# Optimization experiments

Measured on AMD Instinct MI355X. Metric: run time of the kernel, lower is better.

The kernel has to match this reference:

```python
import jax, jax.numpy as jnp
import numpy as np

N_SRC, N_TGT, K = 16384, 65536, 8      # coarse nodes, fine nodes, IDW neighbours per target
C, C_SKIP, S, HID = 16, 2, 32, 64      # mv channels (d_model), skip mv channels, scalars, MLP hidden
MV = 16                                # PGA multivector blade dimension


def setup_inputs() -> dict:
    key = jax.random.key(0)
    ks = jax.random.split(key, 11)
    E = N_TGT * K
    return {
        'mv_src': jax.random.normal(ks[0], (N_SRC, C, MV), jnp.float32),
        'mv_skip': jax.random.normal(ks[1], (N_TGT, C_SKIP, MV), jnp.float32),
        'sc_src': jax.random.normal(ks[2], (N_SRC, S), jnp.float32),
        'sc_skip': jax.random.normal(ks[3], (N_TGT, S), jnp.float32),
        'pos_src': jax.random.uniform(ks[4], (N_SRC, 3), jnp.float32),
        'pos_tgt': jax.random.uniform(ks[5], (N_TGT, 3), jnp.float32),
        'interp_source': jax.random.randint(ks[6], (E,), 0, N_SRC, dtype=jnp.int32),
        # every target receives exactly K source contributions (sorted, like torch_geometric knn edges)
        'interp_target': jnp.repeat(jnp.arange(N_TGT, dtype=jnp.int32), K),
        'W1_mv': jax.random.normal(ks[7], (C + C_SKIP, HID), jnp.float32) / np.float32(np.sqrt(C + C_SKIP)),
        'W2_mv': jax.random.normal(ks[8], (HID, C), jnp.float32) / np.float32(np.sqrt(HID)),
        'W1_s': jax.random.normal(ks[9], (2 * S, HID), jnp.float32) / np.float32(np.sqrt(2 * S)),
        'b1_s': jnp.zeros((HID,), jnp.float32),
        'W2_s': jax.random.normal(ks[10], (HID, S), jnp.float32) / np.float32(np.sqrt(HID)),
        'b2_s': jnp.zeros((S,), jnp.float32),
    }


def _interp(mv_src, mv_skip, sc_src, sc_skip, pos_src, pos_tgt,
            interp_source, interp_target, W1_mv, W2_mv, W1_s, b1_s, W2_s, b2_s):
    # --- inverse-distance-weighted interpolation (gather -> weight -> scatter-sum) ---
    pos_diff = pos_src[interp_source] - pos_tgt[interp_target]            # [E,3]
    d2 = jnp.clip(jnp.sum(pos_diff * pos_diff, axis=-1), 1e-16)           # [E]
    w = 1.0 / d2                                                          # IDW weight
    denom = jax.ops.segment_sum(w, interp_target, num_segments=N_TGT)     # [N_tgt]
    mv = jax.ops.segment_sum(mv_src[interp_source] * w[:, None, None],
                             interp_target, num_segments=N_TGT) / denom[:, None, None]
    sc = jax.ops.segment_sum(sc_src[interp_source] * w[:, None],
                             interp_target, num_segments=N_TGT) / denom[:, None]
    # --- skip concat (torch.cat dim=-2 for multivectors, dim=-1 for scalars) ---
    mv = jnp.concatenate((mv, mv_skip), axis=-2)                          # [N_tgt, C+C_SKIP, 16]
    sc = jnp.concatenate((sc, sc_skip), axis=-1)                          # [N_tgt, 2S]
    # --- equivariant MLP: channel-mixing linear on multivectors (blade-wise), gated scalar path ---
    mv_h = jnp.einsum('nci,ch->nhi', mv, W1_mv)                           # [N_tgt, HID, 16]
    sc_h = jax.nn.gelu(sc @ W1_s + b1_s)                                  # [N_tgt, HID]
    mv_o = jnp.einsum('nhi,hc->nci', mv_h, W2_mv)                         # [N_tgt, C, 16]
    sc_o = sc_h @ W2_s + b2_s                                             # [N_tgt, S]
    return mv_o, sc_o


def reference(mv_src, mv_skip, sc_src, sc_skip, pos_src, pos_tgt,
              interp_source, interp_target, W1_mv, W2_mv, W1_s, b1_s, W2_s, b2_s):
    return _interp(mv_src, mv_skip, sc_src, sc_skip, pos_src, pos_tgt,
                   interp_source, interp_target, W1_mv, W2_mv, W1_s, b1_s, W2_s, b2_s)
```

## Files before the change

### kernel.cpp

```cpp
#include <hip/hip_runtime.h>
#include <hip/hip_fp16.h>

#define N_SRC 16384
#define N_TGT 65536
#define KNN 8
#define CMV 16
#define CSKIP 2
#define SSC 32
#define HID 64
#define MVD 16

#define OUT_MV_ELEMS (N_TGT * CMV * MVD)
#define PROJ_OFFSET 512

__device__ __forceinline__ float gelu_tanh(float x) {
    const float k0 = 0.7978845608028654f;
    const float k1 = 0.044715f;
    float yy = k0 * (x + k1 * x * x * x);
    return 0.5f * x * (1.0f + tanhf(yy));
}

__global__ __launch_bounds__(256) void kA_preproject(
        const float* __restrict__ mv_src,
        const float* __restrict__ W1_mv,
        const float* __restrict__ W2_mv,
        float* __restrict__ ws) {
    __shared__ float sWeff[CMV][MVD];
    int tid = threadIdx.x;
    {
        int c = tid >> 4, d = tid & 15;
        float a = 0.f;
        #pragma unroll 8
        for (int h = 0; h < HID; ++h)
            a = fmaf(W1_mv[c * HID + h], W2_mv[h * MVD + d], a);
        sWeff[c][d] = a;
    }
    if (blockIdx.x == 0 && tid < 32) {
        int j = tid >> 4, d = tid & 15;
        float a = 0.f;
        #pragma unroll 8
        for (int h = 0; h < HID; ++h)
            a = fmaf(W1_mv[(CMV + j) * HID + h], W2_mv[h * MVD + d], a);
        ws[j * MVD + d] = a;
    }
    __syncthreads();

    int lane = tid & 63;
    int d = lane >> 2, q = lane & 3;
    float wcol[CMV];
    #pragma unroll
    for (int c = 0; c < CMV; ++c) wcol[c] = sWeff[c][d];

    __half* proj = (__half*)(ws + PROJ_OFFSET);
    int wid = (int)((blockIdx.x * blockDim.x + tid) >> 6);
    int nw  = (int)((gridDim.x * blockDim.x) >> 6);
    for (int s = wid; s < N_SRC; s += nw) {
        const float* row = mv_src + (size_t)s * 256;
        float4 o = make_float4(0.f, 0.f, 0.f, 0.f);
        #pragma unroll
        for (int c = 0; c < CMV; ++c) {
            float4 v = *(const float4*)(row + c * 16 + q * 4);
            o.x = fmaf(v.x, wcol[c], o.x);
            o.y = fmaf(v.y, wcol[c], o.y);
            o.z = fmaf(v.z, wcol[c], o.z);
            o.w = fmaf(v.w, wcol[c], o.w);
        }
        union { __half2 h[2]; uint2 u; } P;
        P.h[0] = __floats2half2_rn(o.x, o.y);
        P.h[1] = __floats2half2_rn(o.z, o.w);
        *(uint2*)(proj + (size_t)s * 256 + lane * 4) = P.u;
    }
}

__global__ __launch_bounds__(256, 6) void kB_mv(
        const float* __restrict__ ws,
        const float* __restrict__ mv_skip,
        const float* __restrict__ pos_src,
        const float* __restrict__ pos_tgt,
        const int*   __restrict__ isrc,
        float* __restrict__ out) {
    int tid = threadIdx.x;
    int lane = tid & 63;
    int d = lane >> 2, q = lane & 3;
    float wsk0 = ws[d];
    float wsk1 = ws[MVD + d];
    const __half* proj = (const __half*)(ws + PROJ_OFFSET);

    int wid = (int)((blockIdx.x * blockDim.x + tid) >> 6);
    int t0 = wid * 8;

    #pragma unroll
    for (int pp = 0; pp < 4; ++pp) {
        int tA = t0 + pp * 2, tB = tA + 1;
        float wA = 0.f, wB = 0.f; int sA = 0, sB = 0;
        if (lane < KNN) {
            sA = isrc[tA * KNN + lane];
            sB = isrc[tB * KNN + lane];
            float ax = pos_src[sA * 3 + 0] - pos_tgt[tA * 3 + 0];
            float ay = pos_src[sA * 3 + 1] - pos_tgt[tA * 3 + 1];
            float az = pos_src[sA * 3 + 2] - pos_tgt[tA * 3 + 2];
            float bx = pos_src[sB * 3 + 0] - pos_tgt[tB * 3 + 0];
            float by = pos_src[sB * 3 + 1] - pos_tgt[tB * 3 + 1];
            float bz = pos_src[sB * 3 + 2] - pos_tgt[tB * 3 + 2];
            float dA = fmaxf(ax * ax + ay * ay + az * az, 1e-16f);
            float dB = fmaxf(bx * bx + by * by + bz * bz, 1e-16f);
            wA = 1.0f / dA;
            wB = 1.0f / dB;
        }
        float denA = wA, denB = wB;
        denA += __shfl_xor(denA, 1); denB += __shfl_xor(denB, 1);
        denA += __shfl_xor(denA, 2); denB += __shfl_xor(denB, 2);
        denA += __shfl_xor(denA, 4); denB += __shfl_xor(denB, 4);
        float wnA = wA / denA, wnB = wB / denB;

        uint2 g[16];
        #pragma unroll
        for (int k = 0; k < KNN; ++k) {
            int sk = __builtin_amdgcn_readlane(sA, k);
            g[k] = *(const uint2*)(proj + (size_t)sk * 256 + lane * 4);
        }
        #pragma unroll
        for (int k = 0; k < KNN; ++k) {
            int sk = __builtin_amdgcn_readlane(sB, k);
            g[8 + k] = *(const uint2*)(proj + (size_t)sk * 256 + lane * 4);
        }

        float4 accA = make_float4(0.f, 0.f, 0.f, 0.f);
        float4 accB = make_float4(0.f, 0.f, 0.f, 0.f);
        #pragma unroll
        for (int k = 0; k < KNN; ++k) {
            float wk = __uint_as_float(
                __builtin_amdgcn_readlane(__float_as_uint(wnA), k));
            union { uint2 u; __half2 h[2]; } P; P.u = g[k];
            float2 lo = __half22float2(P.h[0]);
            float2 hi = __half22float2(P.h[1]);
            accA.x = fmaf(wk, lo.x, accA.x);
            accA.y = fmaf(wk, lo.y, accA.y);
            accA.z = fmaf(wk, hi.x, accA.z);
            accA.w = fmaf(wk, hi.y, accA.w);
        }
        #pragma unroll
        for (int k = 0; k < KNN; ++k) {
            float wk = __uint_as_float(
                __builtin_amdgcn_readlane(__float_as_uint(wnB), k));
            union { uint2 u; __half2 h[2]; } P; P.u = g[8 + k];
            float2 lo = __half22float2(P.h[0]);
            float2 hi = __half22float2(P.h[1]);
            accB.x = fmaf(wk, lo.x, accB.x);
            accB.y = fmaf(wk, lo.y, accB.y);
            accB.z = fmaf(wk, hi.x, accB.z);
            accB.w = fmaf(wk, hi.y, accB.w);
        }

        {
            const float4 u0 = *(const float4*)(mv_skip + (size_t)tA * 32 + q * 4);
            const float4 u1 = *(const float4*)(mv_skip + (size_t)tA * 32 + 16 + q * 4);
            float4 o;
            o.x = accA.x + fmaf(wsk0, u0.x, wsk1 * u1.x);
            o.y = accA.y + fmaf(wsk0, u0.y, wsk1 * u1.y);
            o.z = accA.z + fmaf(wsk0, u0.z, wsk1 * u1.z);
            o.w = accA.w + fmaf(wsk0, u0.w, wsk1 * u1.w);
            *(float4*)(out + (size_t)tA * 256 + lane * 4) = o;
        }
        {
            const float4 u0 = *(const float4*)(mv_skip + (size_t)tB * 32 + q * 4);
            const float4 u1 = *(const float4*)(mv_skip + (size_t)tB * 32 + 16 + q * 4);
            float4 o;
            o.x = accB.x + fmaf(wsk0, u0.x, wsk1 * u1.x);
            o.y = accB.y + fmaf(wsk0, u0.y, wsk1 * u1.y);
            o.z = accB.z + fmaf(wsk0, u0.z, wsk1 * u1.z);
            o.w = accB.w + fmaf(wsk0, u0.w, wsk1 * u1.w);
            *(float4*)(out + (size_t)tB * 256 + lane * 4) = o;
        }
    }
}

__global__ __launch_bounds__(256) void kBf_mv(
        const float* __restrict__ mv_src,
        const float* __restrict__ mv_skip,
        const float* __restrict__ pos_src,
        const float* __restrict__ pos_tgt,
        const int*   __restrict__ isrc,
        const float* __restrict__ W1_mv,
        const float* __restrict__ W2_mv,
        float* __restrict__ out) {
    __shared__ float sWeff[CMV + CSKIP][MVD];
    __shared__ float stage[4][256];
    int tid = threadIdx.x;
    for (int e = tid; e < (CMV + CSKIP) * MVD; e += 256) {
        int c = e >> 4, d = e & 15;
        float a = 0.f;
        #pragma unroll 8
        for (int h = 0; h < HID; ++h)
            a = fmaf(W1_mv[c * HID + h], W2_mv[h * MVD + d], a);
        sWeff[c][d] = a;
    }
    __syncthreads();

    int lane = tid & 63, wv = tid >> 6;
    int d = lane >> 2, q = lane & 3;
    float wcol[CMV + CSKIP];
    #pragma unroll
    for (int c = 0; c < CMV + CSKIP; ++c) wcol[c] = sWeff[c][d];

    int wid = (int)((blockIdx.x * blockDim.x + tid) >> 6);
    int nw  = (int)((gridDim.x * blockDim.x) >> 6);
    for (int t = wid; t < N_TGT; t += nw) {
        float w = 0.f; int src = 0;
        if (lane < KNN) {
            src = isrc[t * KNN + lane];
            float dx = pos_src[src * 3 + 0] - pos_tgt[t * 3 + 0];
            float dy = pos_src[src * 3 + 1] - pos_tgt[t * 3 + 1];
            float dz = pos_src[src * 3 + 2] - pos_tgt[t * 3 + 2];
            float d2 = fmaxf(dx * dx + dy * dy + dz * dz, 1e-16f);
            w = 1.0f / d2;
        }
        float denom = w;
        denom += __shfl_xor(denom, 1);
        denom += __shfl_xor(denom, 2);
        denom += __shfl_xor(denom, 4);
        denom = __shfl(denom, 0);
        float invd = 1.0f / denom;

        float4 acc = make_float4(0.f, 0.f, 0.f, 0.f);
        #pragma unroll
        for (int k = 0; k < KNN; ++k) {
            int   sk = __builtin_amdgcn_readlane(src, k);
            float wk = __uint_as_float(__builtin_amdgcn_readlane(__float_as_uint(w), k));
            float4 v = *(const float4*)(mv_src + (size_t)sk * 256 + lane * 4);
            acc.x = fmaf(wk, v.x, acc.x);
            acc.y = fmaf(wk, v.y, acc.y);
            acc.z = fmaf(wk, v.z, acc.z);
            acc.w = fmaf(wk, v.w, acc.w);
        }
        asm volatile("" ::: "memory");
        *(float4*)&stage[wv][lane * 4] = acc;
        asm volatile("s_waitcnt lgkmcnt(0)" ::: "memory");
        __builtin_amdgcn_sched_barrier(0);

        float4 o = make_float4(0.f, 0.f, 0.f, 0.f);
        #pragma unroll
        for (int c = 0; c < CMV; ++c) {
            float4 v = *(const float4*)&stage[wv][c * 16 + q * 4];
            o.x = fmaf(v.x, wcol[c], o.x);
            o.y = fmaf(v.y, wcol[c], o.y);
            o.z = fmaf(v.z, wcol[c], o.z);
            o.w = fmaf(v.w, wcol[c], o.w);
        }
        const float4 u0 = *(const float4*)(mv_skip + (size_t)t * 32 + q * 4);
        const float4 u1 = *(const float4*)(mv_skip + (size_t)t * 32 + 16 + q * 4);
        float4 r;
        r.x = fmaf(o.x, invd, fmaf(wcol[16], u0.x, wcol[17] * u1.x));
        r.y = fmaf(o.y, invd, fmaf(wcol[16], u0.y, wcol[17] * u1.y));
        r.z = fmaf(o.z, invd, fmaf(wcol[16], u0.z, wcol[17] * u1.z));
        r.w = fmaf(o.w, invd, fmaf(wcol[16], u0.w, wcol[17] * u1.w));
        *(float4*)(out + (size_t)t * 256 + lane * 4) = r;
    }
}

__global__ __launch_bounds__(256) void kC_scalar(
        const float* __restrict__ sc_src,
        const float* __restrict__ sc_skip,
        const float* __restrict__ pos_src,
        const float* __restrict__ pos_tgt,
        const int*   __restrict__ isrc,
        const float* __restrict__ W1_s,
        const float* __restrict__ b1_s,
        const float* __restrict__ W2_s,
        const float* __restrict__ b2_s,
        float* __restrict__ out) {
    __shared__ float sW1[HID * HID];
    __shared__ float sW2T[SSC][68];
    __shared__ float sXT[HID][68];
    __shared__ float sH[64][68];
    __shared__ float swgt[64][9];
    __shared__ int   ssrcl[64][9];
    __shared__ float sb1[HID], sb2[SSC];

    int tid = threadIdx.x;
    #pragma unroll
    for (int r = 0; r < 4; ++r) {
        float4 v = *(const float4*)(W1_s + (r * 256 + tid) * 4);
        *(float4*)&sW1[(r * 256 + tid) * 4] = v;
    }
    for (int e = tid; e < HID * SSC; e += 256) {
        int h = e >> 5, s = e & 31;
        sW2T[s][h] = W2_s[e];
    }
    if (tid < HID) sb1[tid] = b1_s[tid];
    else if (tid < HID + SSC) sb2[tid - HID] = b2_s[tid - HID];

    int t0 = blockIdx.x * 64;
    if (tid < 64) {
        int t = t0 + tid;
        float ptx = pos_tgt[t * 3 + 0], pty = pos_tgt[t * 3 + 1], ptz = pos_tgt[t * 3 + 2];
        int4 e0 = *(const int4*)(isrc + t * KNN);
        int4 e1 = *(const int4*)(isrc + t * KNN + 4);
        int sk[KNN] = {e0.x, e0.y, e0.z, e0.w, e1.x, e1.y, e1.z, e1.w};
        float wk[KNN];
        float denom = 0.f;
        #pragma unroll
        for (int k = 0; k < KNN; ++k) {
            int s = sk[k];
            float dx = pos_src[s * 3 + 0] - ptx;
            float dy = pos_src[s * 3 + 1] - pty;
            float dz = pos_src[s * 3 + 2] - ptz;
            float d2 = fmaxf(dx * dx + dy * dy + dz * dz, 1e-16f);
            wk[k] = 1.0f / d2;
            denom += wk[k];
        }
        float invd = 1.0f / denom;
        #pragma unroll
        for (int k = 0; k < KNN; ++k) {
            swgt[tid][k] = wk[k] * invd;
            ssrcl[tid][k] = sk[k];
        }
    }
    __syncthreads();

    {
        int wv = tid >> 6, lane = tid & 63;
        int k = lane >> 3;
        int m = lane & 7;
        for (int i = 0; i < 16; i += 4) {
            int tb = wv * 16 + i;
            float4 v[4]; float wn4[4];
            #pragma unroll
            for (int j = 0; j < 4; ++j) {
                int tl = tb + j;
                wn4[j] = swgt[tl][k];
                int sk = ssrcl[tl][k];
                v[j] = *(const float4*)(sc_src + (size_t)sk * SSC + m * 4);
            }
            float4 u;
            if (lane < 32)
                u = *(const float4*)(sc_skip + (size_t)(t0 + tb + k) * SSC + m * 4);
            #pragma unroll
            for (int j = 0; j < 4; ++j) {
                float4 a = v[j]; float wn = wn4[j];
                a.x *= wn; a.y *= wn; a.z *= wn; a.w *= wn;
                #pragma unroll
                for (int sft = 8; sft <= 32; sft <<= 1) {
                    a.x += __shfl_xor(a.x, sft);
                    a.y += __shfl_xor(a.y, sft);
                    a.z += __shfl_xor(a.z, sft);
                    a.w += __shfl_xor(a.w, sft);
                }
                if (lane < 8) {
                    sXT[4 * lane + 0][tb + j] = a.x;
                    sXT[4 * lane + 1][tb + j] = a.y;
                    sXT[4 * lane + 2][tb + j] = a.z;
                    sXT[4 * lane + 3][tb + j] = a.w;
                }
            }
            if (lane < 32) {
                sXT[SSC + 4 * m + 0][tb + k] = u.x;
                sXT[SSC + 4 * m + 1][tb + k] = u.y;
                sXT[SSC + 4 * m + 2][tb + k] = u.z;
                sXT[SSC + 4 * m + 3][tb + k] = u.w;
            }
        }
    }
    __syncthreads();

    int wv = tid >> 6;
    int lane = tid & 63;
    int tr4 = lane >> 4;
    int hc  = lane & 15;
    int tbase = wv * 16 + tr4 * 4;
    float acc[4][4];
    #pragma unroll
    for (int i = 0; i < 4; ++i)
        #pragma unroll
        for (int j = 0; j < 4; ++j) acc[i][j] = 0.f;

    #pragma unroll 2
    for (int c = 0; c < HID; ++c) {
        float4 xv = *(const float4*)&sXT[c][tbase];
        float4 wv4 = *(const float4*)&sW1[c * HID + hc * 4];
        acc[0][0] = fmaf(xv.x, wv4.x, acc[0][0]);
        acc[0][1] = fmaf(xv.x, wv4.y, acc[0][1]);
        acc[0][2] = fmaf(xv.x, wv4.z, acc[0][2]);
        acc[0][3] = fmaf(xv.x, wv4.w, acc[0][3]);
        acc[1][0] = fmaf(xv.y, wv4.x, acc[1][0]);
        acc[1][1] = fmaf(xv.y, wv4.y, acc[1][1]);
        acc[1][2] = fmaf(xv.y, wv4.z, acc[1][2]);
        acc[1][3] = fmaf(xv.y, wv4.w, acc[1][3]);
        acc[2][0] = fmaf(xv.z, wv4.x, acc[2][0]);
        acc[2][1] = fmaf(xv.z, wv4.y, acc[2][1]);
        acc[2][2] = fmaf(xv.z, wv4.z, acc[2][2]);
        acc[2][3] = fmaf(xv.z, wv4.w, acc[2][3]);
        acc[3][0] = fmaf(xv.w, wv4.x, acc[3][0]);
        acc[3][1] = fmaf(xv.w, wv4.y, acc[3][1]);
        acc[3][2] = fmaf(xv.w, wv4.z, acc[3][2]);
        acc[3][3] = fmaf(xv.w, wv4.w, acc[3][3]);
    }
    {
        float b0 = sb1[hc * 4 + 0], b1 = sb1[hc * 4 + 1];
        float b2 = sb1[hc * 4 + 2], b3 = sb1[hc * 4 + 3];
        #pragma unroll
        for (int i = 0; i < 4; ++i) {
            float4 hv;
            hv.x = gelu_tanh(acc[i][0] + b0);
            hv.y = gelu_tanh(acc[i][1] + b1);
            hv.z = gelu_tanh(acc[i][2] + b2);
            hv.w = gelu_tanh(acc[i][3] + b3);
            *(float4*)&sH[tbase + i][hc * 4] = hv;
        }
    }
    __syncthreads();

    int sc16 = lane & 15;
    float acc2[4][2];
    #pragma unroll
    for (int i = 0; i < 4; ++i) { acc2[i][0] = 0.f; acc2[i][1] = 0.f; }
    #pragma unroll 2
    for (int hh = 0; hh < 16; ++hh) {
        float4 wa = *(const float4*)&sW2T[sc16 * 2 + 0][hh * 4];
        float4 wb = *(const float4*)&sW2T[sc16 * 2 + 1][hh * 4];
        #pragma unroll
        for (int i = 0; i < 4; ++i) {
            float4 hv = *(const float4*)&sH[tbase + i][hh * 4];
            acc2[i][0] = fmaf(hv.x, wa.x, acc2[i][0]);
            acc2[i][0] = fmaf(hv.y, wa.y, acc2[i][0]);
            acc2[i][0] = fmaf(hv.z, wa.z, acc2[i][0]);
            acc2[i][0] = fmaf(hv.w, wa.w, acc2[i][0]);
            acc2[i][1] = fmaf(hv.x, wb.x, acc2[i][1]);
            acc2[i][1] = fmaf(hv.y, wb.y, acc2[i][1]);
            acc2[i][1] = fmaf(hv.z, wb.z, acc2[i][1]);
            acc2[i][1] = fmaf(hv.w, wb.w, acc2[i][1]);
        }
    }
    float* osc = out + OUT_MV_ELEMS;
    float bb0 = sb2[sc16 * 2 + 0], bb1 = sb2[sc16 * 2 + 1];
    #pragma unroll
    for (int i = 0; i < 4; ++i) {
        int t = t0 + tbase + i;
        float2 r = make_float2(acc2[i][0] + bb0, acc2[i][1] + bb1);
        *(float2*)&osc[(size_t)t * SSC + sc16 * 2] = r;
    }
}

extern "C" void kernel_launch(void* const* d_in, const int* in_sizes, int n_in,
                              void* d_out, int out_size, void* d_ws, size_t ws_size,
                              hipStream_t stream) {
    const float* mv_src   = (const float*)d_in[0];
    const float* mv_skip  = (const float*)d_in[1];
    const float* sc_src   = (const float*)d_in[2];
    const float* sc_skip  = (const float*)d_in[3];
    const float* pos_src  = (const float*)d_in[4];
    const float* pos_tgt  = (const float*)d_in[5];
    const int*   isrc     = (const int*)d_in[6];
    const float* W1_mv    = (const float*)d_in[8];
    const float* W2_mv    = (const float*)d_in[9];
    const float* W1_s     = (const float*)d_in[10];
    const float* b1_s     = (const float*)d_in[11];
    const float* W2_s     = (const float*)d_in[12];
    const float* b2_s     = (const float*)d_in[13];
    float* out = (float*)d_out;
    float* ws  = (float*)d_ws;

    size_t need_ws_bytes = PROJ_OFFSET * sizeof(float) + (size_t)N_SRC * 256 * sizeof(__half);
    if (ws_size >= need_ws_bytes) {
        hipLaunchKernelGGL(kA_preproject, dim3(512), dim3(256), 0, stream,
                           mv_src, W1_mv, W2_mv, ws);
        hipLaunchKernelGGL(kB_mv, dim3(2048), dim3(256), 0, stream,
                           ws, mv_skip, pos_src, pos_tgt, isrc, out);
    } else {
        hipLaunchKernelGGL(kBf_mv, dim3(2048), dim3(256), 0, stream,
                           mv_src, mv_skip, pos_src, pos_tgt, isrc, W1_mv, W2_mv, out);
    }
    hipLaunchKernelGGL(kC_scalar, dim3(N_TGT / 64), dim3(256), 0, stream,
                       sc_src, sc_skip, pos_src, pos_tgt, isrc,
                       W1_s, b1_s, W2_s, b2_s, out);
}
```

Measured before the change: 208.6 us.

## Fuse scalar IDW+MLP path into multivector gather kernel with nontemporal streaming

```diff
diff --git a/kernel.cpp b/kernel.cpp
--- a/kernel.cpp
+++ b/kernel.cpp
@@ -13,11 +13,23 @@
 #define OUT_MV_ELEMS (N_TGT * CMV * MVD)
 #define PROJ_OFFSET 512
 
+typedef float vf4 __attribute__((ext_vector_type(4)));
+
+__device__ __forceinline__ float4 nt_load4(const float* p) {
+    vf4 v = __builtin_nontemporal_load((const vf4*)p);
+    return make_float4(v.x, v.y, v.z, v.w);
+}
+__device__ __forceinline__ void nt_store4(float* p, float4 o) {
+    vf4 v; v.x = o.x; v.y = o.y; v.z = o.z; v.w = o.w;
+    __builtin_nontemporal_store(v, (vf4*)p);
+}
+
 __device__ __forceinline__ float gelu_tanh(float x) {
     const float k0 = 0.7978845608028654f;
     const float k1 = 0.044715f;
     float yy = k0 * (x + k1 * x * x * x);
-    return 0.5f * x * (1.0f + tanhf(yy));
+    float e = __expf(2.0f * yy);
+    return 0.5f * x * (2.0f - 2.0f / (e + 1.0f));
 }
 
 __global__ __launch_bounds__(256) void kA_preproject(
@@ -72,46 +84,69 @@
     }
 }
 
-__global__ __launch_bounds__(256, 6) void kB_mv(
+__global__ __launch_bounds__(256) void kBC(
         const float* __restrict__ ws,
         const float* __restrict__ mv_skip,
+        const float* __restrict__ sc_src,
+        const float* __restrict__ sc_skip,
         const float* __restrict__ pos_src,
         const float* __restrict__ pos_tgt,
         const int*   __restrict__ isrc,
+        const float* __restrict__ W1_s,
+        const float* __restrict__ b1_s,
+        const float* __restrict__ W2_s,
+        const float* __restrict__ b2_s,
         float* __restrict__ out) {
+    __shared__ float sW1[HID][HID];
+    __shared__ float sW2T[SSC][HID + 4];
+    __shared__ float sX[4][8][HID];
+    __shared__ float sb1[HID], sb2[SSC];
+
     int tid = threadIdx.x;
-    int lane = tid & 63;
+    for (int e = tid; e < HID * HID; e += 256) sW1[e >> 6][e & 63] = W1_s[e];
+    for (int e = tid; e < HID * SSC; e += 256) { int h = e >> 5, s = e & 31; sW2T[s][h] = W2_s[e]; }
+    if (tid < HID) sb1[tid] = b1_s[tid];
+    else if (tid < HID + SSC) sb2[tid - HID] = b2_s[tid - HID];
+    __syncthreads();
+
+    int lane = tid & 63, wv = tid >> 6;
     int d = lane >> 2, q = lane & 3;
-    float wsk0 = ws[d];
-    float wsk1 = ws[MVD + d];
+    float wsk0 = ws[d], wsk1 = ws[MVD + d];
     const __half* proj = (const __half*)(ws + PROJ_OFFSET);
 
     int wid = (int)((blockIdx.x * blockDim.x + tid) >> 6);
     int t0 = wid * 8;
 
+    int   srcv[8];
+    float wnv[8];
+    #pragma unroll
+    for (int tl = 0; tl < 8; ++tl) {
+        int t = t0 + tl;
+        float w = 0.f; int s = 0;
+        if (lane < KNN) {
+            s = isrc[t * KNN + lane];
+            float dx = pos_src[s * 3 + 0] - pos_tgt[t * 3 + 0];
+            float dy = pos_src[s * 3 + 1] - pos_tgt[t * 3 + 1];
+            float dz = pos_src[s * 3 + 2] - pos_tgt[t * 3 + 2];
+            float d2 = fmaxf(dx * dx + dy * dy + dz * dz, 1e-16f);
+            w = 1.0f / d2;
+        }
+        float den = w;
+        den += __shfl_xor(den, 1);
+        den += __shfl_xor(den, 2);
+        den += __shfl_xor(den, 4);
+        srcv[tl] = s;
+        wnv[tl]  = w / den;
+    }
+
+    int kk = lane >> 3;
+    int mm = lane & 7;
+
     #pragma unroll
     for (int pp = 0; pp < 4; ++pp) {
         int tA = t0 + pp * 2, tB = tA + 1;
-        float wA = 0.f, wB = 0.f; int sA = 0, sB = 0;
-        if (lane < KNN) {
-            sA = isrc[tA * KNN + lane];
-            sB = isrc[tB * KNN + lane];
-            float ax = pos_src[sA * 3 + 0] - pos_tgt[tA * 3 + 0];
-            float ay = pos_src[sA * 3 + 1] - pos_tgt[tA * 3 + 1];
-            float az = pos_src[sA * 3 + 2] - pos_tgt[tA * 3 + 2];
-            float bx = pos_src[sB * 3 + 0] - pos_tgt[tB * 3 + 0];
-            float by = pos_src[sB * 3 + 1] - pos_tgt[tB * 3 + 1];
-            float bz = pos_src[sB * 3 + 2] - pos_tgt[tB * 3 + 2];
-            float dA = fmaxf(ax * ax + ay * ay + az * az, 1e-16f);
-            float dB = fmaxf(bx * bx + by * by + bz * bz, 1e-16f);
-            wA = 1.0f / dA;
-            wB = 1.0f / dB;
-        }
-        float denA = wA, denB = wB;
-        denA += __shfl_xor(denA, 1); denB += __shfl_xor(denB, 1);
-        denA += __shfl_xor(denA, 2); denB += __shfl_xor(denB, 2);
-        denA += __shfl_xor(denA, 4); denB += __shfl_xor(denB, 4);
-        float wnA = wA / denA, wnB = wB / denB;
+        float wnA = wnv[pp * 2], wnB = wnv[pp * 2 + 1];
+        int   sA  = srcv[pp * 2], sB = srcv[pp * 2 + 1];
 
         uint2 g[16];
         #pragma unroll
@@ -125,12 +160,19 @@
             g[8 + k] = *(const uint2*)(proj + (size_t)sk * 256 + lane * 4);
         }
 
+        int   skA = __shfl(sA, kk),  skB = __shfl(sB, kk);
+        float waE = __shfl(wnA, kk), wbE = __shfl(wnB, kk);
+        float4 vA = *(const float4*)(sc_src + (size_t)skA * SSC + mm * 4);
+        float4 vB = *(const float4*)(sc_src + (size_t)skB * SSC + mm * 4);
+        float4 vS = make_float4(0.f, 0.f, 0.f, 0.f);
+        if (lane < 16)
+            vS = nt_load4(sc_skip + (size_t)(tA + (lane >> 3)) * SSC + (lane & 7) * 4);
+
         float4 accA = make_float4(0.f, 0.f, 0.f, 0.f);
         float4 accB = make_float4(0.f, 0.f, 0.f, 0.f);
         #pragma unroll
         for (int k = 0; k < KNN; ++k) {
-            float wk = __uint_as_float(
-                __builtin_amdgcn_readlane(__float_as_uint(wnA), k));
+            float wk = __uint_as_float(__builtin_amdgcn_readlane(__float_as_uint(wnA), k));
             union { uint2 u; __half2 h[2]; } P; P.u = g[k];
             float2 lo = __half22float2(P.h[0]);
             float2 hi = __half22float2(P.h[1]);
@@ -141,8 +183,7 @@
         }
         #pragma unroll
         for (int k = 0; k < KNN; ++k) {
-            float wk = __uint_as_float(
-                __builtin_amdgcn_readlane(__float_as_uint(wnB), k));
+            float wk = __uint_as_float(__builtin_amdgcn_readlane(__float_as_uint(wnB), k));
             union { uint2 u; __half2 h[2]; } P; P.u = g[8 + k];
             float2 lo = __half22float2(P.h[0]);
             float2 hi = __half22float2(P.h[1]);
@@ -152,25 +193,94 @@
             accB.w = fmaf(wk, hi.y, accB.w);
         }
 
+        vA.x *= waE; vA.y *= waE; vA.z *= waE; vA.w *= waE;
+        vB.x *= wbE; vB.y *= wbE; vB.z *= wbE; vB.w *= wbE;
+        #pragma unroll
+        for (int sft = 8; sft <= 32; sft <<= 1) {
+            vA.x += __shfl_xor(vA.x, sft); vA.y += __shfl_xor(vA.y, sft);
+            vA.z += __shfl_xor(vA.z, sft); vA.w += __shfl_xor(vA.w, sft);
+            vB.x += __shfl_xor(vB.x, sft); vB.y += __shfl_xor(vB.y, sft);
+            vB.z += __shfl_xor(vB.z, sft); vB.w += __shfl_xor(vB.w, sft);
+        }
+        if (lane < 8) {
+            *(float4*)&sX[wv][pp * 2 + 0][lane * 4] = vA;
+            *(float4*)&sX[wv][pp * 2 + 1][lane * 4] = vB;
+        }
+        if (lane < 16)
+            *(float4*)&sX[wv][pp * 2 + (lane >> 3)][SSC + (lane & 7) * 4] = vS;
+
         {
-            const float4 u0 = *(const float4*)(mv_skip + (size_t)tA * 32 + q * 4);
-            const float4 u1 = *(const float4*)(mv_skip + (size_t)tA * 32 + 16 + q * 4);
+            const float4 u0 = nt_load4(mv_skip + (size_t)tA * 32 + q * 4);
+            const float4 u1 = nt_load4(mv_skip + (size_t)tA * 32 + 16 + q * 4);
             float4 o;
             o.x = accA.x + fmaf(wsk0, u0.x, wsk1 * u1.x);
             o.y = accA.y + fmaf(wsk0, u0.y, wsk1 * u1.y);
             o.z = accA.z + fmaf(wsk0, u0.z, wsk1 * u1.z);
             o.w = accA.w + fmaf(wsk0, u0.w, wsk1 * u1.w);
-            *(float4*)(out + (size_t)tA * 256 + lane * 4) = o;
+            nt_store4(out + (size_t)tA * 256 + lane * 4, o);
         }
         {
-            const float4 u0 = *(const float4*)(mv_skip + (size_t)tB * 32 + q * 4);
-            const float4 u1 = *(const float4*)(mv_skip + (size_t)tB * 32 + 16 + q * 4);
+            const float4 u0 = nt_load4(mv_skip + (size_t)tB * 32 + q * 4);
+            const float4 u1 = nt_load4(mv_skip + (size_t)tB * 32 + 16 + q * 4);
             float4 o;
             o.x = accB.x + fmaf(wsk0, u0.x, wsk1 * u1.x);
             o.y = accB.y + fmaf(wsk0, u0.y, wsk1 * u1.y);
             o.z = accB.z + fmaf(wsk0, u0.z, wsk1 * u1.z);
             o.w = accB.w + fmaf(wsk0, u0.w, wsk1 * u1.w);
-            *(float4*)(out + (size_t)tB * 256 + lane * 4) = o;
+            nt_store4(out + (size_t)tB * 256 + lane * 4, o);
+        }
+    }
+
+    float acc[8];
+    #pragma unroll
+    for (int t = 0; t < 8; ++t) acc[t] = 0.f;
+    #pragma unroll 4
+    for (int c4 = 0; c4 < 16; ++c4) {
+        float w0 = sW1[c4 * 4 + 0][lane];
+        float w1 = sW1[c4 * 4 + 1][lane];
+        float w2 = sW1[c4 * 4 + 2][lane];
+        float w3 = sW1[c4 * 4 + 3][lane];
+        #pragma unroll
+        for (int t = 0; t < 8; ++t) {
+            float4 x4 = *(const float4*)&sX[wv][t][c4 * 4];
+            acc[t] = fmaf(x4.x, w0, acc[t]);
+            acc[t] = fmaf(x4.y, w1, acc[t]);
+            acc[t] = fmaf(x4.z, w2, acc[t]);
+            acc[t] = fmaf(x4.w, w3, acc[t]);
+        }
+    }
+    {
+        float bb = sb1[lane];
+        #pragma unroll
+        for (int t = 0; t < 8; ++t) {
+            float h = gelu_tanh(acc[t] + bb);
+            sX[wv][t][lane] = h;
+        }
+    }
+
+    {
+        int s = lane & 31, th = lane >> 5;
+        float acc2[4];
+        #pragma unroll
+        for (int i = 0; i < 4; ++i) acc2[i] = 0.f;
+        #pragma unroll 4
+        for (int h4 = 0; h4 < 16; ++h4) {
+            float4 w4 = *(const float4*)&sW2T[s][h4 * 4];
+            #pragma unroll
+            for (int i = 0; i < 4; ++i) {
+                float4 x4 = *(const float4*)&sX[wv][th * 4 + i][h4 * 4];
+                acc2[i] = fmaf(x4.x, w4.x, acc2[i]);
+                acc2[i] = fmaf(x4.y, w4.y, acc2[i]);
+                acc2[i] = fmaf(x4.z, w4.z, acc2[i]);
+                acc2[i] = fmaf(x4.w, w4.w, acc2[i]);
+            }
+        }
+        float* osc = out + OUT_MV_ELEMS;
+        float bo = sb2[s];
+        #pragma unroll
+        for (int i = 0; i < 4; ++i) {
+            int t = t0 + th * 4 + i;
+            __builtin_nontemporal_store(acc2[i] + bo, &osc[(size_t)t * SSC + s]);
         }
     }
 }
@@ -464,13 +574,14 @@
     if (ws_size >= need_ws_bytes) {
         hipLaunchKernelGGL(kA_preproject, dim3(512), dim3(256), 0, stream,
                            mv_src, W1_mv, W2_mv, ws);
-        hipLaunchKernelGGL(kB_mv, dim3(2048), dim3(256), 0, stream,
-                           ws, mv_skip, pos_src, pos_tgt, isrc, out);
+        hipLaunchKernelGGL(kBC, dim3(2048), dim3(256), 0, stream,
+                           ws, mv_skip, sc_src, sc_skip, pos_src, pos_tgt, isrc,
+                           W1_s, b1_s, W2_s, b2_s, out);
     } else {
         hipLaunchKernelGGL(kBf_mv, dim3(2048), dim3(256), 0, stream,
                            mv_src, mv_skip, pos_src, pos_tgt, isrc, W1_mv, W2_mv, out);
-    }
-    hipLaunchKernelGGL(kC_scalar, dim3(N_TGT / 64), dim3(256), 0, stream,
-                       sc_src, sc_skip, pos_src, pos_tgt, isrc,
-                       W1_s, b1_s, W2_s, b2_s, out);
-}
+        hipLaunchKernelGGL(kC_scalar, dim3(N_TGT / 64), dim3(256), 0, stream,
+                           sc_src, sc_skip, pos_src, pos_tgt, isrc,
+                           W1_s, b1_s, W2_s, b2_s, out);
+    }
+}
```

After: 216.8 us. 4.0% more time.

## Software-pipeline kB_mv gathers with double buffering and nontemporal streaming I/O

Applied to the files above, without the earlier changes.

```diff
diff --git a/kernel.cpp b/kernel.cpp
--- a/kernel.cpp
+++ b/kernel.cpp
@@ -12,6 +12,17 @@
 
 #define OUT_MV_ELEMS (N_TGT * CMV * MVD)
 #define PROJ_OFFSET 512
+
+typedef float vf4 __attribute__((ext_vector_type(4)));
+
+__device__ __forceinline__ float4 nt_load4(const float* p) {
+    vf4 v = __builtin_nontemporal_load((const vf4*)p);
+    return make_float4(v.x, v.y, v.z, v.w);
+}
+__device__ __forceinline__ void nt_store4(float* p, float4 o) {
+    vf4 v; v.x = o.x; v.y = o.y; v.z = o.z; v.w = o.w;
+    __builtin_nontemporal_store(v, (vf4*)p);
+}
 
 __device__ __forceinline__ float gelu_tanh(float x) {
     const float k0 = 0.7978845608028654f;
@@ -72,7 +83,63 @@
     }
 }
 
-__global__ __launch_bounds__(256, 6) void kB_mv(
+#define KB_ISSUE(buf, PP) do {                                               \
+    int _sA = srcv[2 * (PP)], _sB = srcv[2 * (PP) + 1];                      \
+    _Pragma("unroll")                                                        \
+    for (int k = 0; k < 8; ++k) {                                            \
+        int _sk = __builtin_amdgcn_readlane(_sA, k);                         \
+        buf[k] = *(const uint2*)(proj + (size_t)_sk * 256 + lane * 4);       \
+    }                                                                        \
+    _Pragma("unroll")                                                        \
+    for (int k = 0; k < 8; ++k) {                                            \
+        int _sk = __builtin_amdgcn_readlane(_sB, k);                         \
+        buf[8 + k] = *(const uint2*)(proj + (size_t)_sk * 256 + lane * 4);   \
+    }                                                                        \
+} while (0)
+
+#define KB_MATHSTORE(buf, PP) do {                                           \
+    float _wnA = wnv[2 * (PP)], _wnB = wnv[2 * (PP) + 1];                    \
+    float4 accA = make_float4(0.f, 0.f, 0.f, 0.f);                           \
+    float4 accB = make_float4(0.f, 0.f, 0.f, 0.f);                           \
+    _Pragma("unroll")                                                        \
+    for (int k = 0; k < 8; ++k) {                                            \
+        float wk = __uint_as_float(                                          \
+            __builtin_amdgcn_readlane(__float_as_uint(_wnA), k));            \
+        union { uint2 u; __half2 h[2]; } P; P.u = buf[k];                    \
+        float2 lo = __half22float2(P.h[0]);                                  \
+        float2 hi = __half22float2(P.h[1]);                                  \
+        accA.x = fmaf(wk, lo.x, accA.x);                                     \
+        accA.y = fmaf(wk, lo.y, accA.y);                                     \
+        accA.z = fmaf(wk, hi.x, accA.z);                                     \
+        accA.w = fmaf(wk, hi.y, accA.w);                                     \
+    }                                                                        \
+    _Pragma("unroll")                                                        \
+    for (int k = 0; k < 8; ++k) {                                            \
+        float wk = __uint_as_float(                                          \
+            __builtin_amdgcn_readlane(__float_as_uint(_wnB), k));            \
+        union { uint2 u; __half2 h[2]; } P; P.u = buf[8 + k];                \
+        float2 lo = __half22float2(P.h[0]);                                  \
+        float2 hi = __half22float2(P.h[1]);                                  \
+        accB.x = fmaf(wk, lo.x, accB.x);                                     \
+        accB.y = fmaf(wk, lo.y, accB.y);                                     \
+        accB.z = fmaf(wk, hi.x, accB.z);                                     \
+        accB.w = fmaf(wk, hi.y, accB.w);                                     \
+    }                                                                        \
+    int _tA = t0 + 2 * (PP), _tB = _tA + 1;                                  \
+    float4 o;                                                                \
+    o.x = accA.x + fmaf(wsk0, u0A.x, wsk1 * u1A.x);                          \
+    o.y = accA.y + fmaf(wsk0, u0A.y, wsk1 * u1A.y);                          \
+    o.z = accA.z + fmaf(wsk0, u0A.z, wsk1 * u1A.z);                          \
+    o.w = accA.w + fmaf(wsk0, u0A.w, wsk1 * u1A.w);                          \
+    nt_store4(out + (size_t)_tA * 256 + lane * 4, o);                        \
+    o.x = accB.x + fmaf(wsk0, u0B.x, wsk1 * u1B.x);                          \
+    o.y = accB.y + fmaf(wsk0, u0B.y, wsk1 * u1B.y);                          \
+    o.z = accB.z + fmaf(wsk0, u0B.z, wsk1 * u1B.z);                          \
+    o.w = accB.w + fmaf(wsk0, u0B.w, wsk1 * u1B.w);                          \
+    nt_store4(out + (size_t)_tB * 256 + lane * 4, o);                        \
+} while (0)
+
+__global__ __launch_bounds__(256, 4) void kB_mv(
         const float* __restrict__ ws,
         const float* __restrict__ mv_skip,
         const float* __restrict__ pos_src,
@@ -81,97 +148,54 @@
         float* __restrict__ out) {
     int tid = threadIdx.x;
     int lane = tid & 63;
-    int d = lane >> 2, q = lane & 3;
-    float wsk0 = ws[d];
-    float wsk1 = ws[MVD + d];
+    int dd = lane >> 2, q = lane & 3;
+    float wsk0 = ws[dd], wsk1 = ws[MVD + dd];
     const __half* proj = (const __half*)(ws + PROJ_OFFSET);
 
     int wid = (int)((blockIdx.x * blockDim.x + tid) >> 6);
     int t0 = wid * 8;
 
+    int   srcv[8];
+    float wnv[8];
+    #pragma unroll
+    for (int tl = 0; tl < 8; ++tl) {
+        int t = t0 + tl;
+        float w = 0.f; int s = 0;
+        if (lane < KNN) {
+            s = isrc[t * KNN + lane];
+            float dx = pos_src[s * 3 + 0] - pos_tgt[t * 3 + 0];
+            float dy = pos_src[s * 3 + 1] - pos_tgt[t * 3 + 1];
+            float dz = pos_src[s * 3 + 2] - pos_tgt[t * 3 + 2];
+            float d2 = fmaxf(dx * dx + dy * dy + dz * dz, 1e-16f);
+            w = 1.0f / d2;
+        }
+        float den = w;
+        den += __shfl_xor(den, 1);
+        den += __shfl_xor(den, 2);
+        den += __shfl_xor(den, 4);
+        srcv[tl] = s;
+        wnv[tl]  = w / den;
+    }
+
+    uint2 gA[16], gB[16];
+    float4 u0A, u1A, u0B, u1B;
+
+    KB_ISSUE(gA, 0);
     #pragma unroll
     for (int pp = 0; pp < 4; ++pp) {
-        int tA = t0 + pp * 2, tB = tA + 1;
-        float wA = 0.f, wB = 0.f; int sA = 0, sB = 0;
-        if (lane < KNN) {
-            sA = isrc[tA * KNN + lane];
-            sB = isrc[tB * KNN + lane];
-            float ax = pos_src[sA * 3 + 0] - pos_tgt[tA * 3 + 0];
-            float ay = pos_src[sA * 3 + 1] - pos_tgt[tA * 3 + 1];
-            float az = pos_src[sA * 3 + 2] - pos_tgt[tA * 3 + 2];
-            float bx = pos_src[sB * 3 + 0] - pos_tgt[tB * 3 + 0];
-            float by = pos_src[sB * 3 + 1] - pos_tgt[tB * 3 + 1];
-            float bz = pos_src[sB * 3 + 2] - pos_tgt[tB * 3 + 2];
-            float dA = fmaxf(ax * ax + ay * ay + az * az, 1e-16f);
-            float dB = fmaxf(bx * bx + by * by + bz * bz, 1e-16f);
-            wA = 1.0f / dA;
-            wB = 1.0f / dB;
-        }
-        float denA = wA, denB = wB;
-        denA += __shfl_xor(denA, 1); denB += __shfl_xor(denB, 1);
-        denA += __shfl_xor(denA, 2); denB += __shfl_xor(denB, 2);
-        denA += __shfl_xor(denA, 4); denB += __shfl_xor(denB, 4);
-        float wnA = wA / denA, wnB = wB / denB;
-
-        uint2 g[16];
-        #pragma unroll
-        for (int k = 0; k < KNN; ++k) {
-            int sk = __builtin_amdgcn_readlane(sA, k);
-            g[k] = *(const uint2*)(proj + (size_t)sk * 256 + lane * 4);
-        }
-        #pragma unroll
-        for (int k = 0; k < KNN; ++k) {
-            int sk = __builtin_amdgcn_readlane(sB, k);
-            g[8 + k] = *(const uint2*)(proj + (size_t)sk * 256 + lane * 4);
-        }
-
-        float4 accA = make_float4(0.f, 0.f, 0.f, 0.f);
-        float4 accB = make_float4(0.f, 0.f, 0.f, 0.f);
-        #pragma unroll
-        for (int k = 0; k < KNN; ++k) {
-            float wk = __uint_as_float(
-                __builtin_amdgcn_readlane(__float_as_uint(wnA), k));
-            union { uint2 u; __half2 h[2]; } P; P.u = g[k];
-            float2 lo = __half22float2(P.h[0]);
-            float2 hi = __half22float2(P.h[1]);
-            accA.x = fmaf(wk, lo.x, accA.x);
-            accA.y = fmaf(wk, lo.y, accA.y);
-            accA.z = fmaf(wk, hi.x, accA.z);
-            accA.w = fmaf(wk, hi.y, accA.w);
-        }
-        #pragma unroll
-        for (int k = 0; k < KNN; ++k) {
-            float wk = __uint_as_float(
-                __builtin_amdgcn_readlane(__float_as_uint(wnB), k));
-            union { uint2 u; __half2 h[2]; } P; P.u = g[8 + k];
-            float2 lo = __half22float2(P.h[0]);
-            float2 hi = __half22float2(P.h[1]);
-            accB.x = fmaf(wk, lo.x, accB.x);
-            accB.y = fmaf(wk, lo.y, accB.y);
-            accB.z = fmaf(wk, hi.x, accB.z);
-            accB.w = fmaf(wk, hi.y, accB.w);
-        }
-
+        if (pp == 0)      KB_ISSUE(gB, 1);
+        else if (pp == 1) KB_ISSUE(gA, 2);
+        else if (pp == 2) KB_ISSUE(gB, 3);
         {
-            const float4 u0 = *(const float4*)(mv_skip + (size_t)tA * 32 + q * 4);
-            const float4 u1 = *(const float4*)(mv_skip + (size_t)tA * 32 + 16 + q * 4);
-            float4 o;
-            o.x = accA.x + fmaf(wsk0, u0.x, wsk1 * u1.x);
-            o.y = accA.y + fmaf(wsk0, u0.y, wsk1 * u1.y);
-            o.z = accA.z + fmaf(wsk0, u0.z, wsk1 * u1.z);
-            o.w = accA.w + fmaf(wsk0, u0.w, wsk1 * u1.w);
-            *(float4*)(out + (size_t)tA * 256 + lane * 4) = o;
-        }
-        {
-            const float4 u0 = *(const float4*)(mv_skip + (size_t)tB * 32 + q * 4);
-            const float4 u1 = *(const float4*)(mv_skip + (size_t)tB * 32 + 16 + q * 4);
-            float4 o;
-            o.x = accB.x + fmaf(wsk0, u0.x, wsk1 * u1.x);
-            o.y = accB.y + fmaf(wsk0, u0.y, wsk1 * u1.y);
-            o.z = accB.z + fmaf(wsk0, u0.z, wsk1 * u1.z);
-            o.w = accB.w + fmaf(wsk0, u0.w, wsk1 * u1.w);
-            *(float4*)(out + (size_t)tB * 256 + lane * 4) = o;
-        }
+            int tA = t0 + 2 * pp, tB = tA + 1;
+            u0A = nt_load4(mv_skip + (size_t)tA * 32 + q * 4);
+            u1A = nt_load4(mv_skip + (size_t)tA * 32 + 16 + q * 4);
+            u0B = nt_load4(mv_skip + (size_t)tB * 32 + q * 4);
+            u1B = nt_load4(mv_skip + (size_t)tB * 32 + 16 + q * 4);
+        }
+        __builtin_amdgcn_sched_barrier(0);
+        if ((pp & 1) == 0) KB_MATHSTORE(gA, pp);
+        else               KB_MATHSTORE(gB, pp);
     }
 }
 
```

Result: slower. 215.2 us (+3.2%).

## Precompute normalized IDW weights once in preproject kernel and share across mv/scalar kernels

Applied to the files above, without the earlier changes.

```diff
diff --git a/kernel.cpp b/kernel.cpp
--- a/kernel.cpp
+++ b/kernel.cpp
@@ -12,6 +12,18 @@
 
 #define OUT_MV_ELEMS (N_TGT * CMV * MVD)
 #define PROJ_OFFSET 512
+#define WN_OFFSET (PROJ_OFFSET + (N_SRC * 256 / 2))
+
+typedef float vf4 __attribute__((ext_vector_type(4)));
+
+__device__ __forceinline__ float4 nt_load4(const float* p) {
+    vf4 v = __builtin_nontemporal_load((const vf4*)p);
+    return make_float4(v.x, v.y, v.z, v.w);
+}
+__device__ __forceinline__ void nt_store4(float* p, float4 o) {
+    vf4 v; v.x = o.x; v.y = o.y; v.z = o.z; v.w = o.w;
+    __builtin_nontemporal_store(v, (vf4*)p);
+}
 
 __device__ __forceinline__ float gelu_tanh(float x) {
     const float k0 = 0.7978845608028654f;
@@ -22,6 +34,9 @@
 
 __global__ __launch_bounds__(256) void kA_preproject(
         const float* __restrict__ mv_src,
+        const float* __restrict__ pos_src,
+        const float* __restrict__ pos_tgt,
+        const int*   __restrict__ isrc,
         const float* __restrict__ W1_mv,
         const float* __restrict__ W2_mv,
         float* __restrict__ ws) {
@@ -43,6 +58,33 @@
             a = fmaf(W1_mv[(CMV + j) * HID + h], W2_mv[h * MVD + d], a);
         ws[j * MVD + d] = a;
     }
+
+    int gid = blockIdx.x * 256 + tid;
+    if (gid < N_TGT) {
+        int t = gid;
+        float ptx = pos_tgt[t * 3 + 0], pty = pos_tgt[t * 3 + 1], ptz = pos_tgt[t * 3 + 2];
+        int4 e0 = *(const int4*)(isrc + t * KNN);
+        int4 e1 = *(const int4*)(isrc + t * KNN + 4);
+        int sk[KNN] = {e0.x, e0.y, e0.z, e0.w, e1.x, e1.y, e1.z, e1.w};
+        float wk[KNN];
+        float den = 0.f;
+        #pragma unroll
+        for (int k = 0; k < KNN; ++k) {
+            int s = sk[k];
+            float dx = pos_src[s * 3 + 0] - ptx;
+            float dy = pos_src[s * 3 + 1] - pty;
+            float dz = pos_src[s * 3 + 2] - ptz;
+            float d2 = fmaxf(dx * dx + dy * dy + dz * dz, 1e-16f);
+            wk[k] = 1.0f / d2;
+            den += wk[k];
+        }
+        float invd = 1.0f / den;
+        float* wn = ws + WN_OFFSET;
+        float4 a = make_float4(wk[0] * invd, wk[1] * invd, wk[2] * invd, wk[3] * invd);
+        float4 b = make_float4(wk[4] * invd, wk[5] * invd, wk[6] * invd, wk[7] * invd);
+        *(float4*)(wn + (size_t)t * 8)     = a;
+        *(float4*)(wn + (size_t)t * 8 + 4) = b;
+    }
     __syncthreads();
 
     int lane = tid & 63;
@@ -75,103 +117,76 @@
 __global__ __launch_bounds__(256, 6) void kB_mv(
         const float* __restrict__ ws,
         const float* __restrict__ mv_skip,
-        const float* __restrict__ pos_src,
-        const float* __restrict__ pos_tgt,
         const int*   __restrict__ isrc,
         float* __restrict__ out) {
     int tid = threadIdx.x;
     int lane = tid & 63;
-    int d = lane >> 2, q = lane & 3;
-    float wsk0 = ws[d];
-    float wsk1 = ws[MVD + d];
+    int dd = lane >> 2, q = lane & 3;
+    float wsk0 = ws[dd], wsk1 = ws[MVD + dd];
     const __half* proj = (const __half*)(ws + PROJ_OFFSET);
+    const float*  wn   = ws + WN_OFFSET;
 
     int wid = (int)((blockIdx.x * blockDim.x + tid) >> 6);
-    int t0 = wid * 8;
-
-    #pragma unroll
-    for (int pp = 0; pp < 4; ++pp) {
-        int tA = t0 + pp * 2, tB = tA + 1;
-        float wA = 0.f, wB = 0.f; int sA = 0, sB = 0;
-        if (lane < KNN) {
-            sA = isrc[tA * KNN + lane];
-            sB = isrc[tB * KNN + lane];
-            float ax = pos_src[sA * 3 + 0] - pos_tgt[tA * 3 + 0];
-            float ay = pos_src[sA * 3 + 1] - pos_tgt[tA * 3 + 1];
-            float az = pos_src[sA * 3 + 2] - pos_tgt[tA * 3 + 2];
-            float bx = pos_src[sB * 3 + 0] - pos_tgt[tB * 3 + 0];
-            float by = pos_src[sB * 3 + 1] - pos_tgt[tB * 3 + 1];
-            float bz = pos_src[sB * 3 + 2] - pos_tgt[tB * 3 + 2];
-            float dA = fmaxf(ax * ax + ay * ay + az * az, 1e-16f);
-            float dB = fmaxf(bx * bx + by * by + bz * bz, 1e-16f);
-            wA = 1.0f / dA;
-            wB = 1.0f / dB;
-        }
-        float denA = wA, denB = wB;
-        denA += __shfl_xor(denA, 1); denB += __shfl_xor(denB, 1);
-        denA += __shfl_xor(denA, 2); denB += __shfl_xor(denB, 2);
-        denA += __shfl_xor(denA, 4); denB += __shfl_xor(denB, 4);
-        float wnA = wA / denA, wnB = wB / denB;
-
-        uint2 g[16];
-        #pragma unroll
-        for (int k = 0; k < KNN; ++k) {
-            int sk = __builtin_amdgcn_readlane(sA, k);
-            g[k] = *(const uint2*)(proj + (size_t)sk * 256 + lane * 4);
-        }
-        #pragma unroll
-        for (int k = 0; k < KNN; ++k) {
-            int sk = __builtin_amdgcn_readlane(sB, k);
-            g[8 + k] = *(const uint2*)(proj + (size_t)sk * 256 + lane * 4);
-        }
-
-        float4 accA = make_float4(0.f, 0.f, 0.f, 0.f);
-        float4 accB = make_float4(0.f, 0.f, 0.f, 0.f);
-        #pragma unroll
-        for (int k = 0; k < KNN; ++k) {
-            float wk = __uint_as_float(
-                __builtin_amdgcn_readlane(__float_as_uint(wnA), k));
-            union { uint2 u; __half2 h[2]; } P; P.u = g[k];
-            float2 lo = __half22float2(P.h[0]);
-            float2 hi = __half22float2(P.h[1]);
-            accA.x = fmaf(wk, lo.x, accA.x);
-            accA.y = fmaf(wk, lo.y, accA.y);
-            accA.z = fmaf(wk, hi.x, accA.z);
-            accA.w = fmaf(wk, hi.y, accA.w);
-        }
-        #pragma unroll
-        for (int k = 0; k < KNN; ++k) {
-            float wk = __uint_as_float(
-                __builtin_amdgcn_readlane(__float_as_uint(wnB), k));
-            union { uint2 u; __half2 h[2]; } P; P.u = g[8 + k];
-            float2 lo = __half22float2(P.h[0]);
-            float2 hi = __half22float2(P.h[1]);
-            accB.x = fmaf(wk, lo.x, accB.x);
-            accB.y = fmaf(wk, lo.y, accB.y);
-            accB.z = fmaf(wk, hi.x, accB.z);
-            accB.w = fmaf(wk, hi.y, accB.w);
-        }
-
-        {
-            const float4 u0 = *(const float4*)(mv_skip + (size_t)tA * 32 + q * 4);
-            const float4 u1 = *(const float4*)(mv_skip + (size_t)tA * 32 + 16 + q * 4);
-            float4 o;
-            o.x = accA.x + fmaf(wsk0, u0.x, wsk1 * u1.x);
-            o.y = accA.y + fmaf(wsk0, u0.y, wsk1 * u1.y);
-            o.z = accA.z + fmaf(wsk0, u0.z, wsk1 * u1.z);
-            o.w = accA.w + fmaf(wsk0, u0.w, wsk1 * u1.w);
-            *(float4*)(out + (size_t)tA * 256 + lane * 4) = o;
-        }
-        {
-            const float4 u0 = *(const float4*)(mv_skip + (size_t)tB * 32 + q * 4);
-            const float4 u1 = *(const float4*)(mv_skip + (size_t)tB * 32 + 16 + q * 4);
-            float4 o;
-            o.x = accB.x + fmaf(wsk0, u0.x, wsk1 * u1.x);
-            o.y = accB.y + fmaf(wsk0, u0.y, wsk1 * u1.y);
-            o.z = accB.z + fmaf(wsk0, u0.z, wsk1 * u1.z);
-            o.w = accB.w + fmaf(wsk0, u0.w, wsk1 * u1.w);
-            *(float4*)(out + (size_t)tB * 256 + lane * 4) = o;
-        }
+    int t0 = wid * 2;
+
+    int   src2 = 0; float wn2 = 0.f;
+    if (lane < 16) {
+        src2 = isrc[(size_t)t0 * KNN + lane];
+        wn2  = wn[(size_t)t0 * KNN + lane];
+    }
+
+    float4 u0A = nt_load4(mv_skip + (size_t)t0 * 32 + q * 4);
+    float4 u1A = nt_load4(mv_skip + (size_t)t0 * 32 + 16 + q * 4);
+    float4 u0B = nt_load4(mv_skip + (size_t)(t0 + 1) * 32 + q * 4);
+    float4 u1B = nt_load4(mv_skip + (size_t)(t0 + 1) * 32 + 16 + q * 4);
+
+    uint2 g[16];
+    #pragma unroll
+    for (int k = 0; k < 16; ++k) {
+        int sk = __builtin_amdgcn_readlane(src2, k);
+        g[k] = *(const uint2*)(proj + (size_t)sk * 256 + lane * 4);
+    }
+
+    float4 accA = make_float4(0.f, 0.f, 0.f, 0.f);
+    float4 accB = make_float4(0.f, 0.f, 0.f, 0.f);
+    #pragma unroll
+    for (int k = 0; k < KNN; ++k) {
+        float wk = __uint_as_float(__builtin_amdgcn_readlane(__float_as_uint(wn2), k));
+        union { uint2 u; __half2 h[2]; } P; P.u = g[k];
+        float2 lo = __half22float2(P.h[0]);
+        float2 hi = __half22float2(P.h[1]);
+        accA.x = fmaf(wk, lo.x, accA.x);
+        accA.y = fmaf(wk, lo.y, accA.y);
+        accA.z = fmaf(wk, hi.x, accA.z);
+        accA.w = fmaf(wk, hi.y, accA.w);
+    }
+    #pragma unroll
+    for (int k = 0; k < KNN; ++k) {
+        float wk = __uint_as_float(__builtin_amdgcn_readlane(__float_as_uint(wn2), 8 + k));
+        union { uint2 u; __half2 h[2]; } P; P.u = g[8 + k];
+        float2 lo = __half22float2(P.h[0]);
+        float2 hi = __half22float2(P.h[1]);
+        accB.x = fmaf(wk, lo.x, accB.x);
+        accB.y = fmaf(wk, lo.y, accB.y);
+        accB.z = fmaf(wk, hi.x, accB.z);
+        accB.w = fmaf(wk, hi.y, accB.w);
+    }
+
+    {
+        float4 o;
+        o.x = accA.x + fmaf(wsk0, u0A.x, wsk1 * u1A.x);
+        o.y = accA.y + fmaf(wsk0, u0A.y, wsk1 * u1A.y);
+        o.z = accA.z + fmaf(wsk0, u0A.z, wsk1 * u1A.z);
+        o.w = accA.w + fmaf(wsk0, u0A.w, wsk1 * u1A.w);
+        nt_store4(out + (size_t)t0 * 256 + lane * 4, o);
+    }
+    {
+        float4 o;
+        o.x = accB.x + fmaf(wsk0, u0B.x, wsk1 * u1B.x);
+        o.y = accB.y + fmaf(wsk0, u0B.y, wsk1 * u1B.y);
+        o.z = accB.z + fmaf(wsk0, u0B.z, wsk1 * u1B.z);
+        o.w = accB.w + fmaf(wsk0, u0B.w, wsk1 * u1B.w);
+        nt_store4(out + (size_t)(t0 + 1) * 256 + lane * 4, o);
     }
 }
 
@@ -264,6 +279,7 @@
         const float* __restrict__ pos_src,
         const float* __restrict__ pos_tgt,
         const int*   __restrict__ isrc,
+        const float* __restrict__ wn,
         const float* __restrict__ W1_s,
         const float* __restrict__ b1_s,
         const float* __restrict__ W2_s,
@@ -293,26 +309,35 @@
     int t0 = blockIdx.x * 64;
     if (tid < 64) {
         int t = t0 + tid;
-        float ptx = pos_tgt[t * 3 + 0], pty = pos_tgt[t * 3 + 1], ptz = pos_tgt[t * 3 + 2];
         int4 e0 = *(const int4*)(isrc + t * KNN);
         int4 e1 = *(const int4*)(isrc + t * KNN + 4);
         int sk[KNN] = {e0.x, e0.y, e0.z, e0.w, e1.x, e1.y, e1.z, e1.w};
-        float wk[KNN];
-        float denom = 0.f;
+        float wkn[KNN];
+        if (wn) {
+            float4 a = *(const float4*)(wn + (size_t)t * 8);
+            float4 b = *(const float4*)(wn + (size_t)t * 8 + 4);
+            wkn[0] = a.x; wkn[1] = a.y; wkn[2] = a.z; wkn[3] = a.w;
+            wkn[4] = b.x; wkn[5] = b.y; wkn[6] = b.z; wkn[7] = b.w;
+        } else {
+            float ptx = pos_tgt[t * 3 + 0], pty = pos_tgt[t * 3 + 1], ptz = pos_tgt[t * 3 + 2];
+            float den = 0.f;
+            #pragma unroll
+            for (int k = 0; k < KNN; ++k) {
+                int s = sk[k];
+                float dx = pos_src[s * 3 + 0] - ptx;
+                float dy = pos_src[s * 3 + 1] - pty;
+                float dz = pos_src[s * 3 + 2] - ptz;
+                float d2 = fmaxf(dx * dx + dy * dy + dz * dz, 1e-16f);
+                wkn[k] = 1.0f / d2;
+                den += wkn[k];
+            }
+            float invd = 1.0f / den;
+            #pragma unroll
+            for (int k = 0; k < KNN; ++k) wkn[k] *= invd;
+        }
         #pragma unroll
         for (int k = 0; k < KNN; ++k) {
-            int s = sk[k];
-            float dx = pos_src[s * 3 + 0] - ptx;
-            float dy = pos_src[s * 3 + 1] - pty;
-            float dz = pos_src[s * 3 + 2] - ptz;
-            float d2 = fmaxf(dx * dx + dy * dy + dz * dz, 1e-16f);
-            wk[k] = 1.0f / d2;
-            denom += wk[k];
-        }
-        float invd = 1.0f / denom;
-        #pragma unroll
-        for (int k = 0; k < KNN; ++k) {
-            swgt[tid][k] = wk[k] * invd;
+            swgt[tid][k]  = wkn[k];
             ssrcl[tid][k] = sk[k];
         }
     }
@@ -337,8 +362,8 @@
                 u = *(const float4*)(sc_skip + (size_t)(t0 + tb + k) * SSC + m * 4);
             #pragma unroll
             for (int j = 0; j < 4; ++j) {
-                float4 a = v[j]; float wn = wn4[j];
-                a.x *= wn; a.y *= wn; a.z *= wn; a.w *= wn;
+                float4 a = v[j]; float wnj = wn4[j];
+                a.x *= wnj; a.y *= wnj; a.z *= wnj; a.w *= wnj;
                 #pragma unroll
                 for (int sft = 8; sft <= 32; sft <<= 1) {
                     a.x += __shfl_xor(a.x, sft);
@@ -460,17 +485,20 @@
     float* out = (float*)d_out;
     float* ws  = (float*)d_ws;
 
-    size_t need_ws_bytes = PROJ_OFFSET * sizeof(float) + (size_t)N_SRC * 256 * sizeof(__half);
+    size_t need_ws_bytes = (size_t)(WN_OFFSET + (size_t)N_TGT * KNN) * sizeof(float);
     if (ws_size >= need_ws_bytes) {
         hipLaunchKernelGGL(kA_preproject, dim3(512), dim3(256), 0, stream,
-                           mv_src, W1_mv, W2_mv, ws);
-        hipLaunchKernelGGL(kB_mv, dim3(2048), dim3(256), 0, stream,
-                           ws, mv_skip, pos_src, pos_tgt, isrc, out);
+                           mv_src, pos_src, pos_tgt, isrc, W1_mv, W2_mv, ws);
+        hipLaunchKernelGGL(kB_mv, dim3(8192), dim3(256), 0, stream,
+                           ws, mv_skip, isrc, out);
+        hipLaunchKernelGGL(kC_scalar, dim3(N_TGT / 64), dim3(256), 0, stream,
+                           sc_src, sc_skip, pos_src, pos_tgt, isrc, ws + WN_OFFSET,
+                           W1_s, b1_s, W2_s, b2_s, out);
     } else {
         hipLaunchKernelGGL(kBf_mv, dim3(2048), dim3(256), 0, stream,
                            mv_src, mv_skip, pos_src, pos_tgt, isrc, W1_mv, W2_mv, out);
-    }
-    hipLaunchKernelGGL(kC_scalar, dim3(N_TGT / 64), dim3(256), 0, stream,
-                       sc_src, sc_skip, pos_src, pos_tgt, isrc,
-                       W1_s, b1_s, W2_s, b2_s, out);
-}
+        hipLaunchKernelGGL(kC_scalar, dim3(N_TGT / 64), dim3(256), 0, stream,
+                           sc_src, sc_skip, pos_src, pos_tgt, isrc, (const float*)nullptr,
+                           W1_s, b1_s, W2_s, b2_s, out);
+    }
+}
```

After: 201.0 us. 3.6% less time.
